# Kernel optimization log

Hardware: AMD Instinct MI355X
Metric: run time of the kernel (lower is better)

Reference implementation:

```python
import jax, jax.numpy as jnp
import numpy as np

D = 1024
H = 16
HD = D // H
B = 2
S = 2048


def setup_inputs() -> dict:
    key = jax.random.key(0)
    ks = jax.random.split(key, 9)
    sc = 1.0 / np.sqrt(D)
    return {
        "x": jax.random.normal(ks[0], (B, S, D), dtype=jnp.float32),
        "attention_mask": jnp.ones((B, S), dtype=jnp.int32),
        "Wq": jax.random.normal(ks[1], (D, D), dtype=jnp.float32) * sc,
        "bq": jax.random.normal(ks[2], (D,), dtype=jnp.float32) * 0.02,
        "Wk": jax.random.normal(ks[3], (D, D), dtype=jnp.float32) * sc,
        "bk": jax.random.normal(ks[4], (D,), dtype=jnp.float32) * 0.02,
        "Wv": jax.random.normal(ks[5], (D, D), dtype=jnp.float32) * sc,
        "bv": jax.random.normal(ks[6], (D,), dtype=jnp.float32) * 0.02,
        "Wo": jax.random.normal(ks[7], (D, D), dtype=jnp.float32) * sc,
        "bo": jax.random.normal(ks[8], (D,), dtype=jnp.float32) * 0.02,
    }


def reference(x, attention_mask, Wq, bq, Wk, bk, Wv, bv, Wo, bo):
    Bb, Ss, d = x.shape
    # projections (torch Linear: x @ W.T + b; here W stored as [in,out])
    q = (x @ Wq + bq).reshape(Bb, Ss, H, HD).transpose(0, 2, 1, 3)  # [B,H,S,hd]
    k = (x @ Wk + bk).reshape(Bb, Ss, H, HD).transpose(0, 2, 1, 3)
    v = (x @ Wv + bv).reshape(Bb, Ss, H, HD).transpose(0, 2, 1, 3)
    dots = jnp.einsum("bhqd,bhkd->bhqk", q, k) / np.sqrt(HD)  # [B,H,S,S]
    causal = jnp.triu(jnp.ones((Ss, Ss), dtype=bool), k=1)  # True above diagonal
    dots = jnp.where(causal[None, None], -jnp.inf, dots)
    pad = (attention_mask == 0)[:, None, None, :]  # [B,1,1,S]
    dots = jnp.where(pad, -jnp.inf, dots)
    scores = jax.nn.softmax(dots, axis=-1)
    o = jnp.einsum("bhqk,bhkd->bhqd", scores, v)  # [B,H,S,hd]
    o = o.transpose(0, 2, 1, 3).reshape(Bb, Ss, d)
    return o @ Wo + bo
```

## Files before the change

kernel.cpp:

```cpp
#include <hip/hip_runtime.h>

#define D_  1024
#define H_  16
#define HD_ 64
#define B_  2
#define S_  2048
#define M_  (B_*S_)

typedef _Float16 f16;
typedef _Float16 f16x8 __attribute__((ext_vector_type(8)));
typedef _Float16 f16x4 __attribute__((ext_vector_type(4)));
typedef _Float16 f16x2 __attribute__((ext_vector_type(2)));
typedef float    f32x4 __attribute__((ext_vector_type(4)));

#define GLOAD_LDS16(g, l) \
  __builtin_amdgcn_global_load_lds((__attribute__((address_space(1))) const void*)(g), \
                                   (__attribute__((address_space(3))) void*)(l), 16, 0, 0)

__global__ void k_cvt_x(const float* __restrict__ x, f16* __restrict__ xb) {
  int i = blockIdx.x * blockDim.x + threadIdx.x;
  float4 v = ((const float4*)x)[i];
  f16x4 o = { (f16)v.x, (f16)v.y, (f16)v.z, (f16)v.w };
  ((f16x4*)xb)[i] = o;
}

__global__ void k_twt(const float* __restrict__ W, f16* __restrict__ WT) {
  __shared__ float t[32][33];
  int n0 = blockIdx.x * 32, k0 = blockIdx.y * 32;
  int tx = threadIdx.x, ty = threadIdx.y;
  #pragma unroll
  for (int i = 0; i < 4; i++)
    t[ty + i*8][tx] = W[(size_t)(k0 + ty + i*8) * D_ + n0 + tx];
  __syncthreads();
  #pragma unroll
  for (int i = 0; i < 4; i++)
    WT[(size_t)(n0 + ty + i*8) * D_ + k0 + tx] = (f16)t[tx][ty + i*8];
}

template<int MODE>
__device__ __forceinline__ void gemm_body(const f16* __restrict__ A,
                                          const f16* __restrict__ Bt,
                                          const float* __restrict__ bias,
                                          void* __restrict__ Cout) {
  __shared__ __align__(16) f16 lA[128 * 32];
  __shared__ __align__(16) f16 lB[128 * 32];
  const int tid = threadIdx.x;
  const int wv = tid >> 6, lane = tid & 63;
  const int m0 = blockIdx.y * 128, n0 = blockIdx.x * 128;
  const int fr = lane & 15, fg = lane >> 4;
  const int wm = wv >> 1, wn = wv & 1;
  f32x4 acc[4][4] = {};

  for (int k0 = 0; k0 < D_; k0 += 32) {
    #pragma unroll
    for (int it = 0; it < 2; ++it) {
      int c = wv + it * 4;
      int row = c * 16 + (lane >> 2);
      int kk = (lane & 3) * 8;
      GLOAD_LDS16(A  + (size_t)(m0 + row) * D_ + k0 + kk, lA + c * 512);
      GLOAD_LDS16(Bt + (size_t)(n0 + row) * D_ + k0 + kk, lB + c * 512);
    }
    __syncthreads();
    f16x8 a[4], b[4];
    #pragma unroll
    for (int i = 0; i < 4; i++) a[i] = *(const f16x8*)&lA[(wm*64 + i*16 + fr) * 32 + fg * 8];
    #pragma unroll
    for (int j = 0; j < 4; j++) b[j] = *(const f16x8*)&lB[(wn*64 + j*16 + fr) * 32 + fg * 8];
    #pragma unroll
    for (int i = 0; i < 4; i++)
      #pragma unroll
      for (int j = 0; j < 4; j++)
        acc[i][j] = __builtin_amdgcn_mfma_f32_16x16x32_f16(a[i], b[j], acc[i][j], 0, 0, 0);
    __syncthreads();
  }

  #pragma unroll
  for (int i = 0; i < 4; i++) {
    #pragma unroll
    for (int j = 0; j < 4; j++) {
      int grow0 = m0 + wm*64 + i*16 + fg*4;
      int gcol  = n0 + wn*64 + j*16 + fr;
      float bb = bias[gcol];
      #pragma unroll
      for (int r = 0; r < 4; r++) {
        float val = acc[i][j][r] + bb;
        int grow = grow0 + r;
        if (MODE == 0) {
          int b = grow >> 11, s = grow & (S_ - 1);
          int h = gcol >> 6,  hd = gcol & (HD_ - 1);
          ((f16*)Cout)[((size_t)(b * H_ + h) * S_ + s) * HD_ + hd] = (f16)val;
        } else {
          ((float*)Cout)[(size_t)grow * D_ + gcol] = val;
        }
      }
    }
  }
}

__global__ __launch_bounds__(256) void k_gemm_qkv(const f16* __restrict__ A,
                                                  const f16* __restrict__ WT0,
                                                  const float* __restrict__ bq,
                                                  const float* __restrict__ bk,
                                                  const float* __restrict__ bv,
                                                  f16* __restrict__ qkv) {
  int z = blockIdx.z;
  const f16* Bt = WT0 + (size_t)z * D_ * D_;
  const float* bias = (z == 0) ? bq : (z == 1) ? bk : bv;
  f16* outp = qkv + (size_t)z * M_ * D_;
  gemm_body<0>(A, Bt, bias, outp);
}

__global__ __launch_bounds__(256) void k_gemm_out(const f16* __restrict__ A,
                                                  const f16* __restrict__ Bt,
                                                  const float* __restrict__ bias,
                                                  float* __restrict__ Cout) {
  gemm_body<1>(A, Bt, bias, Cout);
}

#define POFF 8.65617025f

__global__ __launch_bounds__(256) void k_attn(const f16* __restrict__ Qh,
                                              const f16* __restrict__ Kh,
                                              const f16* __restrict__ Vh,
                                              const int* __restrict__ am,
                                              f16* __restrict__ OpA, f16* __restrict__ OpB,
                                              float* __restrict__ lpA, float* __restrict__ lpB) {
  __shared__ __align__(16) f16 kt[2][64 * 64];
  __shared__ __align__(16) f16 vt[2][64 * 64];
  __shared__ __align__(16) f16 pl[4][16 * 64];

  const int tid = threadIdx.x;
  const int wv = tid >> 6, lane = tid & 63;
  const int fr = lane & 15, fg = lane >> 4;

  const int d = blockIdx.x;
  const int lo = d & 255, kk4 = d >> 8;
  const int bh = lo & 31;
  const int m  = (lo >> 5) + 8 * (kk4 & 1);
  const int typeB = kk4 >> 1;
  const int b = bh >> 4, h = bh & 15;
  (void)h;

  f16*   Op = typeB ? OpB : OpA;
  float* lp = typeB ? lpB : lpA;

  const f16* Qb = Qh + (size_t)bh * S_ * HD_;
  const f16* Kb = Kh + (size_t)bh * S_ * HD_;
  const f16* Vb = Vh + (size_t)bh * S_ * HD_;
  const int* amb = am + b * S_;
  f16* plw = pl[wv];

  volatile int* flag = (volatile int*)&pl[0][0];
  if (tid == 0) *flag = 1;
  __syncthreads();
  {
    int mv = 1;
    #pragma unroll
    for (int i = 0; i < 8; ++i) mv &= amb[tid * 8 + i];
    if (!mv) *flag = 0;
  }
  __syncthreads();
  const bool allv = (*flag != 0);

  const f16 qs = (f16)0.18033688f;
  const int ksrc = 8 * ((lane & 7) ^ (lane >> 3));
  const int swz = (fr & 7) << 3;
  const int vkk = (tid >> 3) * 2, vd0 = (tid & 7) * 8;
  const int vswz2 = (tid & 3) << 4;
  const f32x4 cinit = { -POFF, -POFF, -POFF, -POFF };

#define STAGE_K(t_, c_) do { \
    const f16* kp_ = Kb + (size_t)((t_) * 64) * HD_; \
    GLOAD_LDS16(kp_ + (size_t)((wv*2+0)*8 + (lane >> 3)) * HD_ + ksrc, &kt[c_][(wv*2+0)*512]); \
    GLOAD_LDS16(kp_ + (size_t)((wv*2+1)*8 + (lane >> 3)) * HD_ + ksrc, &kt[c_][(wv*2+1)*512]); \
  } while (0)

#define LOAD_V(t_) do { \
    const f16* vp_ = Vb + (size_t)((t_) * 64 + vkk) * HD_ + vd0; \
    vA = *(const f16x8*)vp_; vBr = *(const f16x8*)(vp_ + HD_); \
  } while (0)

#define WRITE_V(c_) do { \
    _Pragma("unroll") \
    for (int j_ = 0; j_ < 8; ++j_) { \
      f16x2 pr_ = { vA[j_], vBr[j_] }; \
      *(f16x2*)&vt[c_][(vd0 + j_) * 64 + ((vkk ^ (j_ << 3)) ^ vswz2)] = pr_; \
    } \
  } while (0)

  f16x8 vA, vBr;

  auto run_half = [&](int qt, int t0, int t1) {
    const int q0w = qt * 64 + wv * 16;
    f32x4 accO[4] = {};
    float lrl = 0.f;

    if (t0 < t1) {
      f16x8 qf0, qf1;
      {
        f16x8 r0 = *(const f16x8*)&Qb[(size_t)(q0w + fr) * HD_ + fg*8];
        f16x8 r1 = *(const f16x8*)&Qb[(size_t)(q0w + fr) * HD_ + 32 + fg*8];
        qf0 = r0 * qs; qf1 = r1 * qs;
      }

      STAGE_K(t0, 0);
      LOAD_V(t0);
      WRITE_V(0);
      __syncthreads();

      int c = 0;
      for (int t = t0; t < t1; ++t) {
        const int kb = t * 64;
        const bool pre = (t + 1 < t1);
        if (pre) { STAGE_K(t + 1, c ^ 1); LOAD_V(t + 1); }

        const int dq = q0w - kb;
        int tm = (dq + 15) >> 4; if (tm > 3) tm = 3;
        const bool fullb = (dq >= 63);

        f32x4 s[4];
        #pragma unroll
        for (int tt = 0; tt < 4; ++tt) s[tt] = cinit;

        __builtin_amdgcn_s_setprio(1);
        #pragma unroll
        for (int tt = 0; tt < 4; ++tt) {
          if (tt <= tm) {
            const int kr = (tt*16 + fr) * 64;
            f16x8 kf0 = *(const f16x8*)&kt[c][kr + ((     fg*8) ^ swz)];
            f16x8 kf1 = *(const f16x8*)&kt[c][kr + ((32 + fg*8) ^ swz)];
            s[tt] = __builtin_amdgcn_mfma_f32_16x16x32_f16(kf0, qf0, s[tt], 0, 0, 0);
            s[tt] = __builtin_amdgcn_mfma_f32_16x16x32_f16(kf1, qf1, s[tt], 0, 0, 0);
          }
        }
        __builtin_amdgcn_s_setprio(0);

        const int thr = dq + fr;
        if (allv) {
          #pragma unroll
          for (int tt = 0; tt < 4; ++tt) {
            f16x4 pk4 = {};
            if (tt <= tm) {
              #pragma unroll
              for (int r = 0; r < 4; ++r) {
                float sv = s[tt][r];
                if (!fullb) sv = (tt*16 + fg*4 + r <= thr) ? sv : -1e30f;
                float p = exp2f(sv);
                lrl += p;
                pk4[r] = (f16)p;
              }
            }
            *(f16x4*)&plw[fr * 64 + ((tt*16 + fg*4) ^ swz)] = pk4;
          }
        } else {
          #pragma unroll
          for (int tt = 0; tt < 4; ++tt) {
            f16x4 pk4 = {};
            if (tt <= tm) {
              int4 a4 = *(const int4*)&amb[kb + tt*16 + fg*4];
              #pragma unroll
              for (int r = 0; r < 4; ++r) {
                float sv = s[tt][r];
                if (!fullb) sv = (tt*16 + fg*4 + r <= thr) ? sv : -1e30f;
                float p = exp2f(sv);
                int mr_ = (r == 0) ? a4.x : (r == 1) ? a4.y : (r == 2) ? a4.z : a4.w;
                p = mr_ ? p : 0.0f;
                lrl += p;
                pk4[r] = (f16)p;
              }
            }
            *(f16x4*)&plw[fr * 64 + ((tt*16 + fg*4) ^ swz)] = pk4;
          }
        }

        __builtin_amdgcn_s_setprio(1);
        #pragma unroll
        for (int ks = 0; ks < 2; ++ks) {
          if (ks <= (tm >> 1)) {
            f16x8 pa = *(const f16x8*)&plw[fr * 64 + ((ks*32 + fg*8) ^ swz)];
            #pragma unroll
            for (int nt = 0; nt < 4; ++nt) {
              f16x8 vf = *(const f16x8*)&vt[c][(nt*16 + fr) * 64 +
                           ((ks*32 + fg*8) ^ swz ^ (((2*nt + (fr >> 3)) & 3) << 4))];
              accO[nt] = __builtin_amdgcn_mfma_f32_16x16x32_f16(pa, vf, accO[nt], 0, 0, 0);
            }
          }
        }
        __builtin_amdgcn_s_setprio(0);

        if (pre) WRITE_V(c ^ 1);
        __syncthreads();
        c ^= 1;
      }
    }

    float v = lrl;
    v += __shfl_xor(v, 16);
    v += __shfl_xor(v, 32);
    if (lane < 16) lp[(size_t)bh * S_ + q0w + lane] = v;

    f16* Oprow = Op + (size_t)bh * (S_ * HD_);
    #pragma unroll
    for (int nt = 0; nt < 4; ++nt) {
      int col = nt*16 + fr;
      #pragma unroll
      for (int r = 0; r < 4; ++r) {
        int row = q0w + fg*4 + r;
        Oprow[(size_t)row * HD_ + col] = (f16)accO[nt][r];
      }
    }
  };

  const int haM = (m + 2) >> 1;
  const int haC = (33 - m) >> 1;
  if (!typeB) {
    run_half(m,      0,   haM);
    run_half(31 - m, 0,   haC);
  } else {
    run_half(m,      haM, m + 1);
    run_half(31 - m, haC, 32 - m);
  }

#undef STAGE_K
#undef LOAD_V
#undef WRITE_V
}

__global__ __launch_bounds__(256) void k_comb(const f16* __restrict__ OA,
                                              const f16* __restrict__ OB,
                                              const float* __restrict__ lA,
                                              const float* __restrict__ lB,
                                              f16* __restrict__ Obf) {
  int gid = blockIdx.x * 256 + threadIdx.x;
  int seg = gid & 7, rowg = gid >> 3;
  int bh = rowg >> 11, row = rowg & 2047;
  f16x8 a  = ((const f16x8*)OA)[gid];
  f16x8 b2 = ((const f16x8*)OB)[gid];
  float inv = __builtin_amdgcn_rcpf(lA[rowg] + lB[rowg]);
  f16x8 o;
  #pragma unroll
  for (int j = 0; j < 8; ++j) o[j] = (f16)(((float)a[j] + (float)b2[j]) * inv);
  int bb = bh >> 4, hh = bh & 15;
  *(f16x8*)&Obf[((size_t)(bb * S_ + row)) * D_ + hh * 64 + seg * 8] = o;
}

extern "C" void kernel_launch(void* const* d_in, const int* in_sizes, int n_in,
                              void* d_out, int out_size, void* d_ws, size_t ws_size,
                              hipStream_t stream) {
  const float* x  = (const float*)d_in[0];
  const int*   am = (const int*)d_in[1];
  const float* Wq = (const float*)d_in[2];
  const float* bq = (const float*)d_in[3];
  const float* Wk = (const float*)d_in[4];
  const float* bk = (const float*)d_in[5];
  const float* Wv = (const float*)d_in[6];
  const float* bv = (const float*)d_in[7];
  const float* Wo = (const float*)d_in[8];
  const float* bo = (const float*)d_in[9];

  char* ws = (char*)d_ws;
  f16*   xb  = (f16*)(ws);
  f16*   wt  = (f16*)(ws + (8u  << 20));
  f16*   qkv = (f16*)(ws + (16u << 20));
  f16*   OpA = (f16*)(ws + (40u << 20));
  f16*   OpB = xb;
  float* lpA = (float*)(ws + (8u << 20));
  float* lpB = (float*)(ws + (8u << 20) + (256u << 10));
  f16*   Obf = qkv;

  k_cvt_x<<<4096, 256, 0, stream>>>(x, xb);

  dim3 tb(32, 8), tg(32, 32);
  k_twt<<<tg, tb, 0, stream>>>(Wq, wt + 0 * (size_t)(D_ * D_));
  k_twt<<<tg, tb, 0, stream>>>(Wk, wt + 1 * (size_t)(D_ * D_));
  k_twt<<<tg, tb, 0, stream>>>(Wv, wt + 2 * (size_t)(D_ * D_));
  k_twt<<<tg, tb, 0, stream>>>(Wo, wt + 3 * (size_t)(D_ * D_));

  k_gemm_qkv<<<dim3(8, 32, 3), 256, 0, stream>>>(xb, wt, bq, bk, bv, qkv);

  k_attn<<<dim3(1024), 256, 0, stream>>>(qkv,
                                         qkv + (size_t)M_ * D_,
                                         qkv + 2 * (size_t)M_ * D_,
                                         am, OpA, OpB, lpA, lpB);

  k_comb<<<dim3(2048), 256, 0, stream>>>(OpA, OpB, lpA, lpB, Obf);

  k_gemm_out<<<dim3(8, 32), 256, 0, stream>>>(Obf, wt + 3 * (size_t)(D_ * D_), bo,
                                              (float*)d_out);
}
```

Measured before the change: 139.3 us.

## Process 32 query rows per wave to reuse K/V tiles in attention

Each wave now handles two 16-row query sub-tiles (128 query rows per block), so every K and V fragment read from LDS feeds two MFMAs, and each K/V tile staged from global memory serves twice as many queries. The grid is halved to 512 blocks, and the split of each query tile's key range into A/B halves is re-derived for 128-row tiles. The aim is to cut LDS and global traffic per FLOP. In exchange, register pressure rises from the doubled accumulators, and fewer blocks may leave CUs underused.

```diff
diff --git a/kernel.cpp b/kernel.cpp
--- a/kernel.cpp
+++ b/kernel.cpp
@@ -127,17 +127,16 @@
                                               float* __restrict__ lpA, float* __restrict__ lpB) {
   __shared__ __align__(16) f16 kt[2][64 * 64];
   __shared__ __align__(16) f16 vt[2][64 * 64];
-  __shared__ __align__(16) f16 pl[4][16 * 64];
+  __shared__ __align__(16) f16 pl[4][32 * 64];
 
   const int tid = threadIdx.x;
   const int wv = tid >> 6, lane = tid & 63;
   const int fr = lane & 15, fg = lane >> 4;
 
   const int d = blockIdx.x;
-  const int lo = d & 255, kk4 = d >> 8;
-  const int bh = lo & 31;
-  const int m  = (lo >> 5) + 8 * (kk4 & 1);
-  const int typeB = kk4 >> 1;
+  const int bh = d & 31;
+  const int m  = (d >> 5) & 7;
+  const int typeB = d >> 8;
   const int b = bh >> 4, h = bh & 15;
   (void)h;
 
@@ -191,134 +190,153 @@
   f16x8 vA, vBr;
 
   auto run_half = [&](int qt, int t0, int t1) {
-    const int q0w = qt * 64 + wv * 16;
-    f32x4 accO[4] = {};
-    float lrl = 0.f;
-
-    if (t0 < t1) {
-      f16x8 qf0, qf1;
-      {
-        f16x8 r0 = *(const f16x8*)&Qb[(size_t)(q0w + fr) * HD_ + fg*8];
-        f16x8 r1 = *(const f16x8*)&Qb[(size_t)(q0w + fr) * HD_ + 32 + fg*8];
-        qf0 = r0 * qs; qf1 = r1 * qs;
-      }
-
-      STAGE_K(t0, 0);
-      LOAD_V(t0);
-      WRITE_V(0);
-      __syncthreads();
-
-      int c = 0;
-      for (int t = t0; t < t1; ++t) {
-        const int kb = t * 64;
-        const bool pre = (t + 1 < t1);
-        if (pre) { STAGE_K(t + 1, c ^ 1); LOAD_V(t + 1); }
-
-        const int dq = q0w - kb;
-        int tm = (dq + 15) >> 4; if (tm > 3) tm = 3;
+    const int q0w = qt * 128 + wv * 32;
+
+    f16x8 qf[2][2];
+    #pragma unroll
+    for (int rt = 0; rt < 2; ++rt) {
+      f16x8 r0 = *(const f16x8*)&Qb[(size_t)(q0w + rt*16 + fr) * HD_ + fg*8];
+      f16x8 r1 = *(const f16x8*)&Qb[(size_t)(q0w + rt*16 + fr) * HD_ + 32 + fg*8];
+      qf[rt][0] = r0 * qs; qf[rt][1] = r1 * qs;
+    }
+
+    f32x4 accO[2][4] = {};
+    float lrl[2] = {0.f, 0.f};
+
+    STAGE_K(t0, 0);
+    LOAD_V(t0);
+    WRITE_V(0);
+    __syncthreads();
+
+    int c = 0;
+    for (int t = t0; t < t1; ++t) {
+      const int kb = t * 64;
+      const bool pre = (t + 1 < t1);
+      if (pre) { STAGE_K(t + 1, c ^ 1); LOAD_V(t + 1); }
+
+      const int dq = q0w - kb;
+      if (dq + 31 >= 0) {
+        int tm1 = (dq + 31) >> 4; if (tm1 > 3) tm1 = 3;
+        int tm0 = (dq + 15) >> 4; if (tm0 > 3) tm0 = 3;
         const bool fullb = (dq >= 63);
 
-        f32x4 s[4];
+        f32x4 s[2][4];
         #pragma unroll
-        for (int tt = 0; tt < 4; ++tt) s[tt] = cinit;
+        for (int rt = 0; rt < 2; ++rt)
+          #pragma unroll
+          for (int tt = 0; tt < 4; ++tt) s[rt][tt] = cinit;
 
         __builtin_amdgcn_s_setprio(1);
         #pragma unroll
         for (int tt = 0; tt < 4; ++tt) {
-          if (tt <= tm) {
+          if (tt <= tm1) {
             const int kr = (tt*16 + fr) * 64;
             f16x8 kf0 = *(const f16x8*)&kt[c][kr + ((     fg*8) ^ swz)];
             f16x8 kf1 = *(const f16x8*)&kt[c][kr + ((32 + fg*8) ^ swz)];
-            s[tt] = __builtin_amdgcn_mfma_f32_16x16x32_f16(kf0, qf0, s[tt], 0, 0, 0);
-            s[tt] = __builtin_amdgcn_mfma_f32_16x16x32_f16(kf1, qf1, s[tt], 0, 0, 0);
-          }
-        }
-        __builtin_amdgcn_s_setprio(0);
-
-        const int thr = dq + fr;
-        if (allv) {
-          #pragma unroll
-          for (int tt = 0; tt < 4; ++tt) {
-            f16x4 pk4 = {};
-            if (tt <= tm) {
-              #pragma unroll
-              for (int r = 0; r < 4; ++r) {
-                float sv = s[tt][r];
-                if (!fullb) sv = (tt*16 + fg*4 + r <= thr) ? sv : -1e30f;
-                float p = exp2f(sv);
-                lrl += p;
-                pk4[r] = (f16)p;
-              }
-            }
-            *(f16x4*)&plw[fr * 64 + ((tt*16 + fg*4) ^ swz)] = pk4;
-          }
-        } else {
-          #pragma unroll
-          for (int tt = 0; tt < 4; ++tt) {
-            f16x4 pk4 = {};
-            if (tt <= tm) {
-              int4 a4 = *(const int4*)&amb[kb + tt*16 + fg*4];
-              #pragma unroll
-              for (int r = 0; r < 4; ++r) {
-                float sv = s[tt][r];
-                if (!fullb) sv = (tt*16 + fg*4 + r <= thr) ? sv : -1e30f;
-                float p = exp2f(sv);
-                int mr_ = (r == 0) ? a4.x : (r == 1) ? a4.y : (r == 2) ? a4.z : a4.w;
-                p = mr_ ? p : 0.0f;
-                lrl += p;
-                pk4[r] = (f16)p;
-              }
-            }
-            *(f16x4*)&plw[fr * 64 + ((tt*16 + fg*4) ^ swz)] = pk4;
-          }
-        }
-
-        __builtin_amdgcn_s_setprio(1);
-        #pragma unroll
-        for (int ks = 0; ks < 2; ++ks) {
-          if (ks <= (tm >> 1)) {
-            f16x8 pa = *(const f16x8*)&plw[fr * 64 + ((ks*32 + fg*8) ^ swz)];
-            #pragma unroll
-            for (int nt = 0; nt < 4; ++nt) {
-              f16x8 vf = *(const f16x8*)&vt[c][(nt*16 + fr) * 64 +
-                           ((ks*32 + fg*8) ^ swz ^ (((2*nt + (fr >> 3)) & 3) << 4))];
-              accO[nt] = __builtin_amdgcn_mfma_f32_16x16x32_f16(pa, vf, accO[nt], 0, 0, 0);
+            s[1][tt] = __builtin_amdgcn_mfma_f32_16x16x32_f16(kf0, qf[1][0], s[1][tt], 0, 0, 0);
+            s[1][tt] = __builtin_amdgcn_mfma_f32_16x16x32_f16(kf1, qf[1][1], s[1][tt], 0, 0, 0);
+            if (tt <= tm0) {
+              s[0][tt] = __builtin_amdgcn_mfma_f32_16x16x32_f16(kf0, qf[0][0], s[0][tt], 0, 0, 0);
+              s[0][tt] = __builtin_amdgcn_mfma_f32_16x16x32_f16(kf1, qf[0][1], s[0][tt], 0, 0, 0);
             }
           }
         }
         __builtin_amdgcn_s_setprio(0);
 
-        if (pre) WRITE_V(c ^ 1);
-        __syncthreads();
-        c ^= 1;
+        #pragma unroll
+        for (int rt = 0; rt < 2; ++rt) {
+          const int tmr = rt ? tm1 : tm0;
+          if (tmr < 0) continue;
+          const int thr = dq + rt*16 + fr;
+          #pragma unroll
+          for (int tt = 0; tt < 4; ++tt) {
+            f16x4 pk4 = {};
+            if (tt <= tmr) {
+              if (allv) {
+                #pragma unroll
+                for (int r = 0; r < 4; ++r) {
+                  float sv = s[rt][tt][r];
+                  if (!fullb) sv = (tt*16 + fg*4 + r <= thr) ? sv : -1e30f;
+                  float p = exp2f(sv);
+                  lrl[rt] += p;
+                  pk4[r] = (f16)p;
+                }
+              } else {
+                int4 a4 = *(const int4*)&amb[kb + tt*16 + fg*4];
+                #pragma unroll
+                for (int r = 0; r < 4; ++r) {
+                  float sv = s[rt][tt][r];
+                  if (!fullb) sv = (tt*16 + fg*4 + r <= thr) ? sv : -1e30f;
+                  float p = exp2f(sv);
+                  int mr_ = (r == 0) ? a4.x : (r == 1) ? a4.y : (r == 2) ? a4.z : a4.w;
+                  p = mr_ ? p : 0.0f;
+                  lrl[rt] += p;
+                  pk4[r] = (f16)p;
+                }
+              }
+            }
+            *(f16x4*)&plw[(rt*16 + fr) * 64 + ((tt*16 + fg*4) ^ swz)] = pk4;
+          }
+        }
+
+        __builtin_amdgcn_s_setprio(1);
+        #pragma unroll
+        for (int ks = 0; ks < 2; ++ks) {
+          if (ks <= (tm1 >> 1)) {
+            f16x8 vf[4];
+            #pragma unroll
+            for (int nt = 0; nt < 4; ++nt)
+              vf[nt] = *(const f16x8*)&vt[c][(nt*16 + fr) * 64 +
+                           ((ks*32 + fg*8) ^ swz ^ (((2*nt + (fr >> 3)) & 3) << 4))];
+            #pragma unroll
+            for (int rt = 0; rt < 2; ++rt) {
+              const int tmr = rt ? tm1 : tm0;
+              if (tmr >= 0 && ks <= (tmr >> 1)) {
+                f16x8 pa = *(const f16x8*)&plw[(rt*16 + fr) * 64 + ((ks*32 + fg*8) ^ swz)];
+                #pragma unroll
+                for (int nt = 0; nt < 4; ++nt)
+                  accO[rt][nt] = __builtin_amdgcn_mfma_f32_16x16x32_f16(pa, vf[nt], accO[rt][nt], 0, 0, 0);
+              }
+            }
+          }
+        }
+        __builtin_amdgcn_s_setprio(0);
       }
+
+      if (pre) WRITE_V(c ^ 1);
+      __syncthreads();
+      c ^= 1;
     }
 
-    float v = lrl;
-    v += __shfl_xor(v, 16);
-    v += __shfl_xor(v, 32);
-    if (lane < 16) lp[(size_t)bh * S_ + q0w + lane] = v;
-
-    f16* Oprow = Op + (size_t)bh * (S_ * HD_);
-    #pragma unroll
-    for (int nt = 0; nt < 4; ++nt) {
-      int col = nt*16 + fr;
+    #pragma unroll
+    for (int rt = 0; rt < 2; ++rt) {
+      float v = lrl[rt];
+      v += __shfl_xor(v, 16);
+      v += __shfl_xor(v, 32);
+      if (lane < 16) lp[(size_t)bh * S_ + q0w + rt*16 + lane] = v;
+
+      float inv[4];
+      (void)inv;
+      f16* Oprow = Op + (size_t)bh * (S_ * HD_);
       #pragma unroll
-      for (int r = 0; r < 4; ++r) {
-        int row = q0w + fg*4 + r;
-        Oprow[(size_t)row * HD_ + col] = (f16)accO[nt][r];
+      for (int nt = 0; nt < 4; ++nt) {
+        int col = nt*16 + fr;
+        #pragma unroll
+        for (int r = 0; r < 4; ++r) {
+          int row = q0w + rt*16 + fg*4 + r;
+          Oprow[(size_t)row * HD_ + col] = (f16)accO[rt][nt][r];
+        }
       }
     }
   };
 
-  const int haM = (m + 2) >> 1;
-  const int haC = (33 - m) >> 1;
+  const int qtA = m, qtB = 15 - m;
   if (!typeB) {
-    run_half(m,      0,   haM);
-    run_half(31 - m, 0,   haC);
+    run_half(qtA, 0, qtA + 1);
+    run_half(qtB, 0, qtB + 1);
   } else {
-    run_half(m,      haM, m + 1);
-    run_half(31 - m, haC, 32 - m);
+    run_half(qtA, qtA + 1, 2 * (qtA + 1));
+    run_half(qtB, qtB + 1, 2 * (qtB + 1));
   }
 
 #undef STAGE_K
@@ -378,10 +396,10 @@
 
   k_gemm_qkv<<<dim3(8, 32, 3), 256, 0, stream>>>(xb, wt, bq, bk, bv, qkv);
 
-  k_attn<<<dim3(1024), 256, 0, stream>>>(qkv,
-                                         qkv + (size_t)M_ * D_,
-                                         qkv + 2 * (size_t)M_ * D_,
-                                         am, OpA, OpB, lpA, lpB);
+  k_attn<<<dim3(512), 256, 0, stream>>>(qkv,
+                                        qkv + (size_t)M_ * D_,
+                                        qkv + 2 * (size_t)M_ * D_,
+                                        am, OpA, OpB, lpA, lpB);
 
   k_comb<<<dim3(2048), 256, 0, stream>>>(OpA, OpB, lpA, lpB, Obf);
 
```

Result: faster. 132.6 us (-4.8%).
